# Kernel optimization log

Measured on AMD Instinct MI355X. Metric: run time of the kernel, lower is better.

The kernel has to match this reference:

```python
import jax, jax.numpy as jnp
import numpy as np

B, S, D = 4, 4096, 64

def setup_inputs() -> dict:
    key = jax.random.key(0)
    kq, kk, kv = jax.random.split(key, 3)
    q = jax.random.normal(kq, (B, S, D), dtype=jnp.float32)
    k = jax.random.normal(kk, (B, S, D), dtype=jnp.float32)
    v = jax.random.normal(kv, (B, S, D), dtype=jnp.float32)
    return {"q": q, "k": k, "v": v}

def reference(q, k, v):
    d_k = k.shape[-1]
    # scores: [B, S, S]
    scores = jnp.einsum('bqd,bkd->bqk', q, k) / jnp.sqrt(jnp.asarray(d_k, q.dtype))
    s = scores.shape[-1]
    # causal mask: disallow j > i (strict upper triangle)
    causal = jnp.tril(jnp.ones((scores.shape[-2], s), dtype=bool))
    scores = jnp.where(causal, scores, jnp.asarray(-jnp.inf, scores.dtype))
    norm_scores = jax.nn.softmax(scores, axis=-1)
    return jnp.einsum('bqk,bkd->bqd', norm_scores, v)
```

## Files before the change

### kernel.cpp

```cpp
#include <hip/hip_runtime.h>

#define B_ 4
#define S_ 4096
#define D_ 64

typedef __attribute__((ext_vector_type(8))) short short8;
typedef __attribute__((ext_vector_type(4))) float f32x4;
typedef __attribute__((ext_vector_type(4))) int int4v;
typedef unsigned short u16;

__device__ __forceinline__ int pack_bf2(float a, float b) {
  unsigned ua = __float_as_uint(a) + 0x8000u;
  unsigned ub = __float_as_uint(b) + 0x8000u;
  return __builtin_amdgcn_perm(ub, ua, 0x07060302);
}

__global__ __launch_bounds__(256) void cvt_all_k(const float* __restrict__ q,
                                                 const float* __restrict__ k,
                                                 const float* __restrict__ v,
                                                 u16* __restrict__ wsQ,
                                                 u16* __restrict__ wsK,
                                                 u16* __restrict__ wsV) {
  int blk = blockIdx.x;
  if (blk < 1024) {
    const float* src = (blk < 512) ? q : k;
    u16* dst = (blk < 512) ? wsQ : wsK;
    float scale = (blk < 512) ? 0.18033688011112042f : 1.0f;
    int t = ((blk & 511) << 8) + threadIdx.x;
    const f32x4* s4 = (const f32x4*)src;
    f32x4 a = s4[2 * t], b = s4[2 * t + 1];
    int4v r;
    r[0] = pack_bf2(a[0] * scale, a[1] * scale);
    r[1] = pack_bf2(a[2] * scale, a[3] * scale);
    r[2] = pack_bf2(b[0] * scale, b[1] * scale);
    r[3] = pack_bf2(b[2] * scale, b[3] * scale);
    *(int4v*)(dst + 8 * (long)t) = r;
  } else {
    int t = ((blk - 1024) << 8) + threadIdx.x;
    int lane = t & 63;
    int rest = t >> 6;
    int js = rest & 1;  rest >>= 1;
    int nb = rest & 3;  rest >>= 2;
    int c64 = rest & 63;
    int b = rest >> 6;
    int cc = lane & 15, gg = lane >> 4;
    int row = c64 * 64 + js * 32 + gg * 8;
    int d = nb * 16 + cc;
    const float* src = v + ((long)(b * S_ + row)) * D_ + d;
    float e[8];
#pragma unroll
    for (int i = 0; i < 8; i++) e[i] = src[(long)i * D_];
    int4v r;
    r[0] = pack_bf2(e[0], e[1]);
    r[1] = pack_bf2(e[2], e[3]);
    r[2] = pack_bf2(e[4], e[5]);
    r[3] = pack_bf2(e[6], e[7]);
    *(int4v*)(wsV + 8 * (long)t) = r;
  }
}

#define MFMA(a, bb, cc) __builtin_amdgcn_mfma_f32_16x16x32_bf16((a), (bb), (cc), 0, 0, 0)

__global__ __launch_bounds__(256) void attn_k(const u16* __restrict__ wsQ,
                                              const u16* __restrict__ wsK,
                                              const u16* __restrict__ wsV,
                                              float* __restrict__ out) {
  int bid = blockIdx.x;
  int b = bid & 3;
  int tau = 255 - (bid >> 2);
  int q0 = tau << 4;
  int tid = threadIdx.x;
  int w = tid >> 6;
  int lane = tid & 63;
  int c = lane & 15, g = lane >> 4;

  __shared__ float sBuf[4][16][68];
  __shared__ float sML[4][16][2];

  float* PQ = &sBuf[w][0][0];

  const u16* qp = wsQ + ((long)(b * S_ + q0 + c)) * D_ + g * 8;
  short8 qf0 = *(const short8*)qp;
  short8 qf1 = *(const short8*)(qp + 32);

  float m = -INFINITY, l = 0.f;
  f32x4 zz = {0.f, 0.f, 0.f, 0.f};
  f32x4 o0 = zz, o1 = zz, o2 = zz, o3 = zz;

  int nch = (q0 >> 6) + 1;
  for (int ck = w; ck < nch; ck += 4) {
    int kb = ck << 6;
    const u16* kp = wsK + ((long)(b * S_ + kb + c)) * D_ + g * 8;
    short8 k00 = *(const short8*)(kp);
    short8 k01 = *(const short8*)(kp + 32);
    short8 k10 = *(const short8*)(kp + 16 * 64);
    short8 k11 = *(const short8*)(kp + 16 * 64 + 32);
    short8 k20 = *(const short8*)(kp + 32 * 64);
    short8 k21 = *(const short8*)(kp + 32 * 64 + 32);
    short8 k30 = *(const short8*)(kp + 48 * 64);
    short8 k31 = *(const short8*)(kp + 48 * 64 + 32);
    const u16* vp = wsV + ((long)(((b * 64 + ck) * 8) * 64 + lane)) * 8;
    short8 v00 = *(const short8*)(vp);
    short8 v01 = *(const short8*)(vp + 512);
    short8 v10 = *(const short8*)(vp + 1024);
    short8 v11 = *(const short8*)(vp + 1536);
    short8 v20 = *(const short8*)(vp + 2048);
    short8 v21 = *(const short8*)(vp + 2560);
    short8 v30 = *(const short8*)(vp + 3072);
    short8 v31 = *(const short8*)(vp + 3584);

    f32x4 s0 = MFMA(k00, qf0, zz); s0 = MFMA(k01, qf1, s0);
    f32x4 s1 = MFMA(k10, qf0, zz); s1 = MFMA(k11, qf1, s1);
    f32x4 s2 = MFMA(k20, qf0, zz); s2 = MFMA(k21, qf1, s2);
    f32x4 s3 = MFMA(k30, qf0, zz); s3 = MFMA(k31, qf1, s3);

    if (ck == nch - 1) {
      int qq = q0 + c;
      int j0 = kb + g * 4;
#pragma unroll
      for (int r2 = 0; r2 < 4; r2++) {
        if (j0 + r2      > qq) s0[r2] = -1e30f;
        if (j0 + 16 + r2 > qq) s1[r2] = -1e30f;
        if (j0 + 32 + r2 > qq) s2[r2] = -1e30f;
        if (j0 + 48 + r2 > qq) s3[r2] = -1e30f;
      }
    }

    float mx = fmaxf(fmaxf(fmaxf(s0[0], s0[1]), fmaxf(s0[2], s0[3])),
                     fmaxf(fmaxf(s1[0], s1[1]), fmaxf(s1[2], s1[3])));
    mx = fmaxf(mx, fmaxf(fmaxf(fmaxf(s2[0], s2[1]), fmaxf(s2[2], s2[3])),
                         fmaxf(fmaxf(s3[0], s3[1]), fmaxf(s3[2], s3[3]))));
    mx = fmaxf(mx, __shfl_xor(mx, 16));
    mx = fmaxf(mx, __shfl_xor(mx, 32));
    float mn = fmaxf(m, mx);
    float al = exp2f(m - mn);

    float sum = 0.f;
#pragma unroll
    for (int r2 = 0; r2 < 4; r2++) {
      s0[r2] = exp2f(s0[r2] - mn); sum += s0[r2];
      s1[r2] = exp2f(s1[r2] - mn); sum += s1[r2];
      s2[r2] = exp2f(s2[r2] - mn); sum += s2[r2];
      s3[r2] = exp2f(s3[r2] - mn); sum += s3[r2];
    }
    sum += __shfl_xor(sum, 16);
    sum += __shfl_xor(sum, 32);
    l = l * al + sum;
    m = mn;
    o0 *= al; o1 *= al; o2 *= al; o3 *= al;

    *(f32x4*)&PQ[c * 68 + 0  + g * 4] = s0;
    *(f32x4*)&PQ[c * 68 + 16 + g * 4] = s1;
    *(f32x4*)&PQ[c * 68 + 32 + g * 4] = s2;
    *(f32x4*)&PQ[c * 68 + 48 + g * 4] = s3;
    asm volatile("s_waitcnt lgkmcnt(0)" ::: "memory");
    f32x4 pa0 = *(f32x4*)&PQ[c * 68 + g * 8];
    f32x4 pa1 = *(f32x4*)&PQ[c * 68 + g * 8 + 4];
    f32x4 pb0 = *(f32x4*)&PQ[c * 68 + 32 + g * 8];
    f32x4 pb1 = *(f32x4*)&PQ[c * 68 + 32 + g * 8 + 4];
    asm volatile("" ::: "memory");
    int4v pi0, pi1;
    pi0[0] = pack_bf2(pa0[0], pa0[1]);
    pi0[1] = pack_bf2(pa0[2], pa0[3]);
    pi0[2] = pack_bf2(pa1[0], pa1[1]);
    pi0[3] = pack_bf2(pa1[2], pa1[3]);
    pi1[0] = pack_bf2(pb0[0], pb0[1]);
    pi1[1] = pack_bf2(pb0[2], pb0[3]);
    pi1[2] = pack_bf2(pb1[0], pb1[1]);
    pi1[3] = pack_bf2(pb1[2], pb1[3]);
    short8 p0 = __builtin_bit_cast(short8, pi0);
    short8 p1 = __builtin_bit_cast(short8, pi1);
    o0 = MFMA(v00, p0, o0); o0 = MFMA(v01, p1, o0);
    o1 = MFMA(v10, p0, o1); o1 = MFMA(v11, p1, o1);
    o2 = MFMA(v20, p0, o2); o2 = MFMA(v21, p1, o2);
    o3 = MFMA(v30, p0, o3); o3 = MFMA(v31, p1, o3);
  }

  if (g == 0) { sML[w][c][0] = m; sML[w][c][1] = l; }
  *(f32x4*)&PQ[c * 68 + 0  + g * 4] = o0;
  *(f32x4*)&PQ[c * 68 + 16 + g * 4] = o1;
  *(f32x4*)&PQ[c * 68 + 32 + g * 4] = o2;
  *(f32x4*)&PQ[c * 68 + 48 + g * 4] = o3;
  __syncthreads();

  int q = tid >> 4;
  int d4 = tid & 15;
  float mg = fmaxf(fmaxf(sML[0][q][0], sML[1][q][0]), fmaxf(sML[2][q][0], sML[3][q][0]));
  float lg = 0.f;
  f32x4 acc = {0.f, 0.f, 0.f, 0.f};
#pragma unroll
  for (int w2 = 0; w2 < 4; w2++) {
    float a = exp2f(sML[w2][q][0] - mg);
    lg += a * sML[w2][q][1];
    f32x4 part = *(f32x4*)&sBuf[w2][q][d4 * 4];
#pragma unroll
    for (int i = 0; i < 4; i++) acc[i] += a * part[i];
  }
  float inv = 1.f / lg;
  float* op = out + ((long)(b * S_ + q0 + q)) * D_ + d4 * 4;
  *(f32x4*)op = acc * inv;
}

extern "C" void kernel_launch(void* const* d_in, const int* in_sizes, int n_in,
                              void* d_out, int out_size, void* d_ws, size_t ws_size,
                              hipStream_t stream) {
  const float* q = (const float*)d_in[0];
  const float* k = (const float*)d_in[1];
  const float* v = (const float*)d_in[2];
  float* out = (float*)d_out;

  u16* wsQ = (u16*)d_ws;
  u16* wsK = wsQ + (long)B_ * S_ * D_;
  u16* wsV = wsK + (long)B_ * S_ * D_;

  cvt_all_k<<<1536, 256, 0, stream>>>(q, k, v, wsQ, wsK, wsV);
  attn_k<<<1024, 256, 0, stream>>>(wsQ, wsK, wsV, out);
}
```

Baseline: 109.8 us.

## Tile 64 queries per block with 4-way key split-K and separate merge kernel

Each block now handles 64 query rows (four 16-row tiles held in registers) and one quarter of the causal key range, so every loaded K/V chunk is reused across four query tiles. Partial max/sum and bf16 partial outputs go to a workspace, and a new merge kernel combines the four splits. P is packed to bf16 before the LDS round-trip, halving LDS traffic. The trade-offs are higher register pressure (launch bounds of 2 blocks), an extra kernel launch, and extra global traffic plus bf16 rounding in the partial outputs.

Measured after the change: 100.9 us. 8.1% less time.

```diff
diff --git a/kernel.cpp b/kernel.cpp
--- a/kernel.cpp
+++ b/kernel.cpp
@@ -3,13 +3,15 @@
 #define B_ 4
 #define S_ 4096
 #define D_ 64
+#define SLOTF 544
 
 typedef __attribute__((ext_vector_type(8))) short short8;
 typedef __attribute__((ext_vector_type(4))) float f32x4;
 typedef __attribute__((ext_vector_type(4))) int int4v;
+typedef __attribute__((ext_vector_type(2))) unsigned uint2v;
 typedef unsigned short u16;
 
-__device__ __forceinline__ int pack_bf2(float a, float b) {
+__device__ __forceinline__ unsigned pack_bf2(float a, float b) {
   unsigned ua = __float_as_uint(a) + 0x8000u;
   unsigned ub = __float_as_uint(b) + 0x8000u;
   return __builtin_amdgcn_perm(ub, ua, 0x07060302);
@@ -30,10 +32,10 @@
     const f32x4* s4 = (const f32x4*)src;
     f32x4 a = s4[2 * t], b = s4[2 * t + 1];
     int4v r;
-    r[0] = pack_bf2(a[0] * scale, a[1] * scale);
-    r[1] = pack_bf2(a[2] * scale, a[3] * scale);
-    r[2] = pack_bf2(b[0] * scale, b[1] * scale);
-    r[3] = pack_bf2(b[2] * scale, b[3] * scale);
+    r[0] = (int)pack_bf2(a[0] * scale, a[1] * scale);
+    r[1] = (int)pack_bf2(a[2] * scale, a[3] * scale);
+    r[2] = (int)pack_bf2(b[0] * scale, b[1] * scale);
+    r[3] = (int)pack_bf2(b[2] * scale, b[3] * scale);
     *(int4v*)(dst + 8 * (long)t) = r;
   } else {
     int t = ((blk - 1024) << 8) + threadIdx.x;
@@ -51,154 +53,182 @@
 #pragma unroll
     for (int i = 0; i < 8; i++) e[i] = src[(long)i * D_];
     int4v r;
-    r[0] = pack_bf2(e[0], e[1]);
-    r[1] = pack_bf2(e[2], e[3]);
-    r[2] = pack_bf2(e[4], e[5]);
-    r[3] = pack_bf2(e[6], e[7]);
+    r[0] = (int)pack_bf2(e[0], e[1]);
+    r[1] = (int)pack_bf2(e[2], e[3]);
+    r[2] = (int)pack_bf2(e[4], e[5]);
+    r[3] = (int)pack_bf2(e[6], e[7]);
     *(int4v*)(wsV + 8 * (long)t) = r;
   }
 }
 
 #define MFMA(a, bb, cc) __builtin_amdgcn_mfma_f32_16x16x32_bf16((a), (bb), (cc), 0, 0, 0)
 
-__global__ __launch_bounds__(256) void attn_k(const u16* __restrict__ wsQ,
-                                              const u16* __restrict__ wsK,
-                                              const u16* __restrict__ wsV,
-                                              float* __restrict__ out) {
+__global__ __launch_bounds__(256, 2) void attn_k(const u16* __restrict__ wsQ,
+                                                 const u16* __restrict__ wsK,
+                                                 const u16* __restrict__ wsV,
+                                                 float* __restrict__ part) {
   int bid = blockIdx.x;
-  int b = bid & 3;
-  int tau = 255 - (bid >> 2);
-  int q0 = tau << 4;
+  int g   = 63 - (bid >> 4);
+  int b   = (bid >> 2) & 3;
+  int ksq = bid & 3;
   int tid = threadIdx.x;
-  int w = tid >> 6;
-  int lane = tid & 63;
-  int c = lane & 15, g = lane >> 4;
+  int w = tid >> 6, lane = tid & 63, c = lane & 15, g4 = lane >> 4;
+  int ks = ksq * 4 + w;
 
   __shared__ float sBuf[4][16][68];
+  __shared__ float sP[4][2][16][36];
   __shared__ float sML[4][16][2];
 
-  float* PQ = &sBuf[w][0][0];
-
-  const u16* qp = wsQ + ((long)(b * S_ + q0 + c)) * D_ + g * 8;
-  short8 qf0 = *(const short8*)qp;
-  short8 qf1 = *(const short8*)(qp + 32);
-
-  float m = -INFINITY, l = 0.f;
+  short8 qf0[4], qf1[4];
+#pragma unroll
+  for (int t = 0; t < 4; t++) {
+    const u16* qp = wsQ + ((long)(b * S_ + g * 64 + t * 16 + c)) * D_ + g4 * 8;
+    qf0[t] = *(const short8*)qp;
+    qf1[t] = *(const short8*)(qp + 32);
+  }
   f32x4 zz = {0.f, 0.f, 0.f, 0.f};
-  f32x4 o0 = zz, o1 = zz, o2 = zz, o3 = zz;
-
-  int nch = (q0 >> 6) + 1;
-  for (int ck = w; ck < nch; ck += 4) {
-    int kb = ck << 6;
-    const u16* kp = wsK + ((long)(b * S_ + kb + c)) * D_ + g * 8;
-    short8 k00 = *(const short8*)(kp);
-    short8 k01 = *(const short8*)(kp + 32);
-    short8 k10 = *(const short8*)(kp + 16 * 64);
-    short8 k11 = *(const short8*)(kp + 16 * 64 + 32);
-    short8 k20 = *(const short8*)(kp + 32 * 64);
-    short8 k21 = *(const short8*)(kp + 32 * 64 + 32);
-    short8 k30 = *(const short8*)(kp + 48 * 64);
-    short8 k31 = *(const short8*)(kp + 48 * 64 + 32);
-    const u16* vp = wsV + ((long)(((b * 64 + ck) * 8) * 64 + lane)) * 8;
-    short8 v00 = *(const short8*)(vp);
-    short8 v01 = *(const short8*)(vp + 512);
-    short8 v10 = *(const short8*)(vp + 1024);
-    short8 v11 = *(const short8*)(vp + 1536);
-    short8 v20 = *(const short8*)(vp + 2048);
-    short8 v21 = *(const short8*)(vp + 2560);
-    short8 v30 = *(const short8*)(vp + 3072);
-    short8 v31 = *(const short8*)(vp + 3584);
-
-    f32x4 s0 = MFMA(k00, qf0, zz); s0 = MFMA(k01, qf1, s0);
-    f32x4 s1 = MFMA(k10, qf0, zz); s1 = MFMA(k11, qf1, s1);
-    f32x4 s2 = MFMA(k20, qf0, zz); s2 = MFMA(k21, qf1, s2);
-    f32x4 s3 = MFMA(k30, qf0, zz); s3 = MFMA(k31, qf1, s3);
-
-    if (ck == nch - 1) {
-      int qq = q0 + c;
-      int j0 = kb + g * 4;
+  float m[4], l[4];
+  f32x4 o[4][4];
+#pragma unroll
+  for (int t = 0; t < 4; t++) {
+    m[t] = -INFINITY; l[t] = 0.f;
+#pragma unroll
+    for (int n = 0; n < 4; n++) o[t][n] = zz;
+  }
+
+  for (int ck = ks; ck <= g; ck += 16) {
+    const u16* kp = wsK + ((long)(b * S_ + ck * 64 + c)) * D_ + g4 * 8;
+    short8 kf[8];
+#pragma unroll
+    for (int jb = 0; jb < 4; jb++) {
+      kf[jb * 2]     = *(const short8*)(kp + jb * 1024);
+      kf[jb * 2 + 1] = *(const short8*)(kp + jb * 1024 + 32);
+    }
+    const u16* vp = wsV + ((long)((b * 64 + ck) * 8 * 64 + lane)) * 8;
+    short8 vf[8];
+#pragma unroll
+    for (int i = 0; i < 8; i++) vf[i] = *(const short8*)(vp + 512 * i);
+
+#pragma unroll
+    for (int t = 0; t < 4; t++) {
+      f32x4 s0 = MFMA(kf[0], qf0[t], zz); s0 = MFMA(kf[1], qf1[t], s0);
+      f32x4 s1 = MFMA(kf[2], qf0[t], zz); s1 = MFMA(kf[3], qf1[t], s1);
+      f32x4 s2 = MFMA(kf[4], qf0[t], zz); s2 = MFMA(kf[5], qf1[t], s2);
+      f32x4 s3 = MFMA(kf[6], qf0[t], zz); s3 = MFMA(kf[7], qf1[t], s3);
+
+      if (ck == g) {
+        int qq = t * 16 + c;
+        int j0 = g4 * 4;
+#pragma unroll
+        for (int r2 = 0; r2 < 4; r2++) {
+          if (j0 + r2      > qq) s0[r2] = -1e30f;
+          if (j0 + 16 + r2 > qq) s1[r2] = -1e30f;
+          if (j0 + 32 + r2 > qq) s2[r2] = -1e30f;
+          if (j0 + 48 + r2 > qq) s3[r2] = -1e30f;
+        }
+      }
+
+      float mx = fmaxf(fmaxf(fmaxf(s0[0], s0[1]), fmaxf(s0[2], s0[3])),
+                       fmaxf(fmaxf(s1[0], s1[1]), fmaxf(s1[2], s1[3])));
+      mx = fmaxf(mx, fmaxf(fmaxf(fmaxf(s2[0], s2[1]), fmaxf(s2[2], s2[3])),
+                           fmaxf(fmaxf(s3[0], s3[1]), fmaxf(s3[2], s3[3]))));
+      mx = fmaxf(mx, __shfl_xor(mx, 16));
+      mx = fmaxf(mx, __shfl_xor(mx, 32));
+      float mn = fmaxf(m[t], mx);
+      float al = exp2f(m[t] - mn);
+
+      float sum = 0.f;
 #pragma unroll
       for (int r2 = 0; r2 < 4; r2++) {
-        if (j0 + r2      > qq) s0[r2] = -1e30f;
-        if (j0 + 16 + r2 > qq) s1[r2] = -1e30f;
-        if (j0 + 32 + r2 > qq) s2[r2] = -1e30f;
-        if (j0 + 48 + r2 > qq) s3[r2] = -1e30f;
+        s0[r2] = exp2f(s0[r2] - mn); sum += s0[r2];
+        s1[r2] = exp2f(s1[r2] - mn); sum += s1[r2];
+        s2[r2] = exp2f(s2[r2] - mn); sum += s2[r2];
+        s3[r2] = exp2f(s3[r2] - mn); sum += s3[r2];
       }
+      sum += __shfl_xor(sum, 16);
+      sum += __shfl_xor(sum, 32);
+      l[t] = l[t] * al + sum;
+      m[t] = mn;
+#pragma unroll
+      for (int n = 0; n < 4; n++) o[t][n] *= al;
+
+      float* P = &sP[w][t & 1][0][0];
+      uint2v w0 = {pack_bf2(s0[0], s0[1]), pack_bf2(s0[2], s0[3])};
+      uint2v w1 = {pack_bf2(s1[0], s1[1]), pack_bf2(s1[2], s1[3])};
+      uint2v w2 = {pack_bf2(s2[0], s2[1]), pack_bf2(s2[2], s2[3])};
+      uint2v w3 = {pack_bf2(s3[0], s3[1]), pack_bf2(s3[2], s3[3])};
+      *(uint2v*)&P[c * 36 + 2 * g4]      = w0;
+      *(uint2v*)&P[c * 36 + 2 * g4 + 8]  = w1;
+      *(uint2v*)&P[c * 36 + 2 * g4 + 16] = w2;
+      *(uint2v*)&P[c * 36 + 2 * g4 + 24] = w3;
+      asm volatile("s_waitcnt lgkmcnt(0)" ::: "memory");
+      short8 p0 = *(const short8*)&P[c * 36 + 4 * g4];
+      short8 p1 = *(const short8*)&P[c * 36 + 16 + 4 * g4];
+      asm volatile("" ::: "memory");
+      o[t][0] = MFMA(vf[0], p0, o[t][0]); o[t][0] = MFMA(vf[1], p1, o[t][0]);
+      o[t][1] = MFMA(vf[2], p0, o[t][1]); o[t][1] = MFMA(vf[3], p1, o[t][1]);
+      o[t][2] = MFMA(vf[4], p0, o[t][2]); o[t][2] = MFMA(vf[5], p1, o[t][2]);
+      o[t][3] = MFMA(vf[6], p0, o[t][3]); o[t][3] = MFMA(vf[7], p1, o[t][3]);
     }
-
-    float mx = fmaxf(fmaxf(fmaxf(s0[0], s0[1]), fmaxf(s0[2], s0[3])),
-                     fmaxf(fmaxf(s1[0], s1[1]), fmaxf(s1[2], s1[3])));
-    mx = fmaxf(mx, fmaxf(fmaxf(fmaxf(s2[0], s2[1]), fmaxf(s2[2], s2[3])),
-                         fmaxf(fmaxf(s3[0], s3[1]), fmaxf(s3[2], s3[3]))));
-    mx = fmaxf(mx, __shfl_xor(mx, 16));
-    mx = fmaxf(mx, __shfl_xor(mx, 32));
-    float mn = fmaxf(m, mx);
-    float al = exp2f(m - mn);
-
-    float sum = 0.f;
-#pragma unroll
-    for (int r2 = 0; r2 < 4; r2++) {
-      s0[r2] = exp2f(s0[r2] - mn); sum += s0[r2];
-      s1[r2] = exp2f(s1[r2] - mn); sum += s1[r2];
-      s2[r2] = exp2f(s2[r2] - mn); sum += s2[r2];
-      s3[r2] = exp2f(s3[r2] - mn); sum += s3[r2];
+  }
+
+  for (int t = 0; t < 4; t++) {
+    if (g4 == 0) { sML[w][c][0] = m[t]; sML[w][c][1] = l[t]; }
+#pragma unroll
+    for (int n = 0; n < 4; n++)
+      *(f32x4*)&sBuf[w][c][n * 16 + g4 * 4] = o[t][n];
+    __syncthreads();
+
+    int q = tid >> 4, d4 = tid & 15;
+    float M = fmaxf(fmaxf(sML[0][q][0], sML[1][q][0]),
+                    fmaxf(sML[2][q][0], sML[3][q][0]));
+    float L = 0.f;
+    f32x4 acc = {0.f, 0.f, 0.f, 0.f};
+#pragma unroll
+    for (int w2 = 0; w2 < 4; w2++) {
+      float mw = sML[w2][q][0];
+      float a = (mw > -INFINITY) ? exp2f(mw - M) : 0.f;
+      L += a * sML[w2][q][1];
+      f32x4 pv = *(f32x4*)&sBuf[w2][q][d4 * 4];
+#pragma unroll
+      for (int i = 0; i < 4; i++) acc[i] += a * pv[i];
     }
-    sum += __shfl_xor(sum, 16);
-    sum += __shfl_xor(sum, 32);
-    l = l * al + sum;
-    m = mn;
-    o0 *= al; o1 *= al; o2 *= al; o3 *= al;
-
-    *(f32x4*)&PQ[c * 68 + 0  + g * 4] = s0;
-    *(f32x4*)&PQ[c * 68 + 16 + g * 4] = s1;
-    *(f32x4*)&PQ[c * 68 + 32 + g * 4] = s2;
-    *(f32x4*)&PQ[c * 68 + 48 + g * 4] = s3;
-    asm volatile("s_waitcnt lgkmcnt(0)" ::: "memory");
-    f32x4 pa0 = *(f32x4*)&PQ[c * 68 + g * 8];
-    f32x4 pa1 = *(f32x4*)&PQ[c * 68 + g * 8 + 4];
-    f32x4 pb0 = *(f32x4*)&PQ[c * 68 + 32 + g * 8];
-    f32x4 pb1 = *(f32x4*)&PQ[c * 68 + 32 + g * 8 + 4];
-    asm volatile("" ::: "memory");
-    int4v pi0, pi1;
-    pi0[0] = pack_bf2(pa0[0], pa0[1]);
-    pi0[1] = pack_bf2(pa0[2], pa0[3]);
-    pi0[2] = pack_bf2(pa1[0], pa1[1]);
-    pi0[3] = pack_bf2(pa1[2], pa1[3]);
-    pi1[0] = pack_bf2(pb0[0], pb0[1]);
-    pi1[1] = pack_bf2(pb0[2], pb0[3]);
-    pi1[2] = pack_bf2(pb1[0], pb1[1]);
-    pi1[3] = pack_bf2(pb1[2], pb1[3]);
-    short8 p0 = __builtin_bit_cast(short8, pi0);
-    short8 p1 = __builtin_bit_cast(short8, pi1);
-    o0 = MFMA(v00, p0, o0); o0 = MFMA(v01, p1, o0);
-    o1 = MFMA(v10, p0, o1); o1 = MFMA(v11, p1, o1);
-    o2 = MFMA(v20, p0, o2); o2 = MFMA(v21, p1, o2);
-    o3 = MFMA(v30, p0, o3); o3 = MFMA(v31, p1, o3);
-  }
-
-  if (g == 0) { sML[w][c][0] = m; sML[w][c][1] = l; }
-  *(f32x4*)&PQ[c * 68 + 0  + g * 4] = o0;
-  *(f32x4*)&PQ[c * 68 + 16 + g * 4] = o1;
-  *(f32x4*)&PQ[c * 68 + 32 + g * 4] = o2;
-  *(f32x4*)&PQ[c * 68 + 48 + g * 4] = o3;
-  __syncthreads();
-
-  int q = tid >> 4;
-  int d4 = tid & 15;
-  float mg = fmaxf(fmaxf(sML[0][q][0], sML[1][q][0]), fmaxf(sML[2][q][0], sML[3][q][0]));
-  float lg = 0.f;
+    float* sp = part + ((long)((b * 256 + g * 4 + t) * 4 + ksq)) * SLOTF;
+    if (d4 == 0) { sp[q] = M; sp[16 + q] = L; }
+    uint2v pw = {pack_bf2(acc[0], acc[1]), pack_bf2(acc[2], acc[3])};
+    *(uint2v*)((u16*)(sp + 32) + q * 64 + d4 * 4) = pw;
+    __syncthreads();
+  }
+}
+
+__global__ __launch_bounds__(256) void merge_k(const float* __restrict__ part,
+                                               float* __restrict__ out) {
+  int bid = blockIdx.x;
+  int b = bid >> 8, tau = bid & 255;
+  int tid = threadIdx.x, q = tid >> 4, d4 = tid & 15;
+  const float* base = part + (long)bid * (4 * SLOTF);
+  float M = -INFINITY;
+#pragma unroll
+  for (int s = 0; s < 4; s++) M = fmaxf(M, base[s * SLOTF + q]);
+  float L = 0.f;
   f32x4 acc = {0.f, 0.f, 0.f, 0.f};
 #pragma unroll
-  for (int w2 = 0; w2 < 4; w2++) {
-    float a = exp2f(sML[w2][q][0] - mg);
-    lg += a * sML[w2][q][1];
-    f32x4 part = *(f32x4*)&sBuf[w2][q][d4 * 4];
-#pragma unroll
-    for (int i = 0; i < 4; i++) acc[i] += a * part[i];
-  }
-  float inv = 1.f / lg;
-  float* op = out + ((long)(b * S_ + q0 + q)) * D_ + d4 * 4;
-  *(f32x4*)op = acc * inv;
+  for (int s = 0; s < 4; s++) {
+    float ms = base[s * SLOTF + q];
+    float a = (ms > -INFINITY) ? exp2f(ms - M) : 0.f;
+    L += a * base[s * SLOTF + 16 + q];
+    const u16* Op = (const u16*)(base + s * SLOTF + 32) + q * 64 + d4 * 4;
+    uint2v pw = *(const uint2v*)Op;
+    acc[0] += a * __uint_as_float(pw[0] << 16);
+    acc[1] += a * __uint_as_float(pw[0] & 0xffff0000u);
+    acc[2] += a * __uint_as_float(pw[1] << 16);
+    acc[3] += a * __uint_as_float(pw[1] & 0xffff0000u);
+  }
+  float inv = 1.f / L;
+  f32x4 r;
+#pragma unroll
+  for (int i = 0; i < 4; i++) r[i] = acc[i] * inv;
+  *(f32x4*)(out + ((long)(b * S_ + tau * 16 + q)) * D_ + d4 * 4) = r;
 }
 
 extern "C" void kernel_launch(void* const* d_in, const int* in_sizes, int n_in,
@@ -212,7 +242,9 @@
   u16* wsQ = (u16*)d_ws;
   u16* wsK = wsQ + (long)B_ * S_ * D_;
   u16* wsV = wsK + (long)B_ * S_ * D_;
+  float* part = (float*)(wsV + (long)B_ * S_ * D_);
 
   cvt_all_k<<<1536, 256, 0, stream>>>(q, k, v, wsQ, wsK, wsV);
-  attn_k<<<1024, 256, 0, stream>>>(wsQ, wsK, wsV, out);
-}
+  attn_k<<<1024, 256, 0, stream>>>(wsQ, wsK, wsV, part);
+  merge_k<<<1024, 256, 0, stream>>>(part, out);
+}
```
